# Kernel optimization log

Measured on AMD Instinct MI355X. Metric: run time of the kernel, lower is better.

## Reference

```python
import jax, jax.numpy as jnp
import numpy as np

S = 128           # seq_len
B = 256           # input_bits (bits per token, also neurons per head)
H = 16            # num_heads
NB = 12           # n_bits_per_neuron -> LUT size 2^12
PB = 7            # relative-position bits = ceil(log2(max_seq_len))
HEAD_IN = 2 * B + PB   # concat(query, key, rel_pos_bits) = 519
THRESH = H // 2


def setup_inputs() -> dict:
    key = jax.random.key(0)
    k1, k2, k3 = jax.random.split(key, 3)
    tokens = jax.random.randint(k1, (S, B), 0, 2, dtype=jnp.int32)           # binary token bits
    memory = jax.random.normal(k2, (H, B, 2 ** NB), dtype=jnp.float32)       # RAM LUT contents per head/neuron
    connections = jax.random.randint(k3, (H, B, NB), 0, HEAD_IN, dtype=jnp.int32)  # per-neuron input-bit wiring
    return {"tokens": tokens, "memory": memory, "connections": connections}


def reference(tokens, memory, connections):
    idx = jnp.arange(S)
    rel = idx[:, None] - idx[None, :]                         # [S,S] i - j
    mask = (rel >= 0).astype(jnp.int32)                        # causal mask (j <= i)
    relc = jnp.clip(rel, 0, S - 1)
    # relative-distance binary encoding, LSB first: [S,S,PB]
    pos_bits = ((relc[..., None] >> jnp.arange(PB)) & 1).astype(jnp.int32)
    q = jnp.broadcast_to(tokens[:, None, :], (S, S, B))
    k = jnp.broadcast_to(tokens[None, :, :], (S, S, B))
    head_in = jnp.concatenate([q, k, pos_bits], axis=-1)       # [S,S,HEAD_IN]
    # RAM address per (query i, key j, head h, neuron n): pack NB wired bits, LSB first
    addr = jnp.zeros((S, S, H, B), dtype=jnp.int32)
    for b in range(NB):  # tiny fixed loop over bit planes, fully vectorized over S,S,H,B
        addr = addr + (head_in[..., connections[:, :, b]] << b)
    # LUT gather: memory[h, n, addr] -> [S,S,H,B]
    h_idx = jnp.arange(H)[:, None]
    n_idx = jnp.arange(B)[None, :]
    vals = memory[h_idx, n_idx, addr]
    bits = (vals > 0.0).astype(jnp.int32)                      # RAM neuron output bit
    # XOR accumulation over attended keys == masked sum mod 2: [S,H,B]
    head_res = jnp.sum(bits * mask[:, :, None, None], axis=1) % 2
    # majority vote across heads per bit
    ones_count = jnp.sum(head_res, axis=1)                     # [S,B]
    return (ones_count > THRESH).astype(jnp.int32)
```

## Files before the change

kernel.cpp:

```cpp
#include <hip/hip_runtime.h>


#define S 128
#define B 256
#define H 16
#define NB 12

__device__ __forceinline__ unsigned sig(unsigned x) {
    return x ^ ((x >> 3) & 0x70u) ^ ((x >> 6) & 0x70u);
}

__global__ __launch_bounds__(256, 4) void softram_kernel(
    const int* __restrict__ tokens,
    const float* __restrict__ memory,
    const int* __restrict__ connections,
    unsigned char* __restrict__ pc)
{
    const int bid  = blockIdx.x;
    const int g    = bid >> 8;
    const int n    = bid & 255;
    const int tid  = threadIdx.x;
    const int wid  = tid >> 6;
    const int hg   = g * 4 + wid;
    const int lane = tid & 63;

    __shared__ unsigned char  bytetab[4 * 4096];
    __shared__ unsigned int   tokT[8][S];
    __shared__ unsigned short akT[4][S];
    __shared__ unsigned short apt[4][S];
    __shared__ int            conns[4][NB];
    __shared__ unsigned int   parts[4][4];

    const float4* mrow = (const float4*)(memory + ((size_t)(hg * 256 + n) << 12));
    float4 va[16];
    #pragma unroll
    for (int t = 0; t < 16; ++t) va[t] = mrow[lane + 64 * t];

    {
        int i = tid >> 1, half = tid & 1;
        const int4* tp = (const int4*)tokens;
        #pragma unroll
        for (int wl = 0; wl < 4; ++wl) {
            int w = half * 4 + wl;
            unsigned v = 0;
            #pragma unroll
            for (int u = 0; u < 8; ++u) {
                int4 x = tp[i * 64 + w * 8 + u];
                v |= (unsigned)(x.x & 1) << (4 * u + 0);
                v |= (unsigned)(x.y & 1) << (4 * u + 1);
                v |= (unsigned)(x.z & 1) << (4 * u + 2);
                v |= (unsigned)(x.w & 1) << (4 * u + 3);
            }
            tokT[w][i] = v;
        }
    }
    if (tid < 4 * NB) {
        int hh = tid / NB, b = tid - hh * NB;
        conns[hh][b] = connections[(size_t)(g * 4 + hh) * (B * NB) + n * NB + b];
    }
    __syncthreads();

    unsigned qmask = 0, kmask = 0, pmask = 0;
    #pragma unroll
    for (int b = 0; b < NB; ++b) {
        int c = conns[wid][b];
        qmask |= (unsigned)(c < 256) << b;
        kmask |= (unsigned)(c >= 256 && c < 512) << b;
        pmask |= (unsigned)(c >= 512) << b;
    }
    const int qb = __popc(qmask);
    const int kb = __popc(kmask);

    unsigned char* __restrict__ bt = &bytetab[wid << 12];
    unsigned long long rlo = 0, rhi = 0;

    if (pmask == 0) {
        unsigned qcls0 = 0, qcls1 = 0;
        #pragma unroll
        for (int e = 0; e < 2; ++e) {
            int ii = lane + 64 * e;
            unsigned qc = 0, kc = 0;
            int qn = 0, kn = 0;
            #pragma unroll
            for (int b = 0; b < NB; ++b) {
                int c = conns[wid][b];
                if (c < 256) {
                    qc |= ((tokT[c >> 5][ii] >> (c & 31)) & 1u) << qn;
                    ++qn;
                } else {
                    int c2 = c - 256;
                    kc |= ((tokT[c2 >> 5][ii] >> (c2 & 31)) & 1u) << kn;
                    ++kn;
                }
            }
            akT[wid][ii] = (unsigned short)kc;
            if (e == 0) qcls0 = qc; else qcls1 = qc;
        }

        #pragma unroll
        for (int t = 0; t < 16; ++t) {
            float4 v = va[t];
            unsigned p = 4u * (unsigned)(lane + 64 * t);
            unsigned w = (unsigned)(v.x > 0.f)
                       | ((unsigned)(v.y > 0.f) << 8)
                       | ((unsigned)(v.z > 0.f) << 16)
                       | ((unsigned)(v.w > 0.f) << 24);
            *(unsigned*)&bt[sig(p)] = w;
        }

        const bool formA = (qb <= 6);
        const int SBITS  = formA ? qb : kb;
        unsigned apl = 0, aul = 0;
        {
            int scnt = 0, lcnt = 0;
            #pragma unroll
            for (int b = 0; b < NB; ++b) {
                int c = conns[wid][b];
                bool isS = formA ? (c < 256) : (c >= 256);
                if (isS) {
                    apl |= (((unsigned)lane >> scnt) & 1u) << b;
                    ++scnt;
                } else {
                    int p = SBITS + lcnt;
                    if (p < 6) apl |= (((unsigned)lane >> p) & 1u) << b;
                    else       aul |= (((unsigned)lane >> (p - 6)) & 1u) << b;
                    ++lcnt;
                }
            }
        }
        const unsigned spl  = sig(apl);
        const unsigned saul = sig(aul);
        unsigned Wlo = 0, Whi = 0;
        #pragma unroll 8
        for (int it = 0; it < 64; ++it) {
            unsigned sau  = (unsigned)__builtin_amdgcn_readlane((int)saul, it);
            unsigned bitv = bt[sau ^ spl] & 1u;
            unsigned long long Bm = __ballot(bitv != 0u);
            Wlo = (lane == it) ? (unsigned)Bm : Wlo;
            Whi = (lane == it) ? (unsigned)(Bm >> 32) : Whi;
        }

        if (formA) {
            unsigned long long A = 0, cap0 = 0, cap1 = 0;
            for (int s8 = 0; s8 < 8; ++s8) {
                uint4 uk = *(const uint4*)&akT[wid][s8 * 8];
                #pragma unroll
                for (int t = 0; t < 8; ++t) {
                    int j = s8 * 8 + t;
                    unsigned w = ((const unsigned*)&uk)[t >> 1];
                    unsigned widx = (unsigned)__builtin_amdgcn_readfirstlane(
                        (int)((w >> ((t & 1) * 16)) & 0xffffu));
                    unsigned g0 = widx << qb;
                    int lsel = (int)(g0 >> 6);
                    unsigned lo = (unsigned)__builtin_amdgcn_readlane((int)Wlo, lsel);
                    unsigned hi = (unsigned)__builtin_amdgcn_readlane((int)Whi, lsel);
                    A ^= ((((unsigned long long)hi << 32) | lo) >> (g0 & 63u));
                    cap0 = (lane == j) ? A : cap0;
                }
            }
            for (int s8 = 8; s8 < 16; ++s8) {
                uint4 uk = *(const uint4*)&akT[wid][s8 * 8];
                #pragma unroll
                for (int t = 0; t < 8; ++t) {
                    int j = s8 * 8 + t;
                    unsigned w = ((const unsigned*)&uk)[t >> 1];
                    unsigned widx = (unsigned)__builtin_amdgcn_readfirstlane(
                        (int)((w >> ((t & 1) * 16)) & 0xffffu));
                    unsigned g0 = widx << qb;
                    int lsel = (int)(g0 >> 6);
                    unsigned lo = (unsigned)__builtin_amdgcn_readlane((int)Wlo, lsel);
                    unsigned hi = (unsigned)__builtin_amdgcn_readlane((int)Whi, lsel);
                    A ^= ((((unsigned long long)hi << 32) | lo) >> (g0 & 63u));
                    cap1 = (lane == j - 64) ? A : cap1;
                }
            }
            rlo = __ballot(((cap0 >> qcls0) & 1ull) != 0ull);
            rhi = __ballot(((cap1 >> qcls1) & 1ull) != 0ull);
        } else {
            unsigned Cw = 0, cap0 = 0, cap1 = 0;
            for (int s8 = 0; s8 < 8; ++s8) {
                uint4 uk = *(const uint4*)&akT[wid][s8 * 8];
                #pragma unroll
                for (int t = 0; t < 8; ++t) {
                    int j = s8 * 8 + t;
                    unsigned w = ((const unsigned*)&uk)[t >> 1];
                    unsigned widx = (unsigned)__builtin_amdgcn_readfirstlane(
                        (int)((w >> ((t & 1) * 16)) & 0xffffu));
                    Cw ^= 1u << widx;
                    cap0 = (lane == j) ? Cw : cap0;
                }
            }
            for (int s8 = 8; s8 < 16; ++s8) {
                uint4 uk = *(const uint4*)&akT[wid][s8 * 8];
                #pragma unroll
                for (int t = 0; t < 8; ++t) {
                    int j = s8 * 8 + t;
                    unsigned w = ((const unsigned*)&uk)[t >> 1];
                    unsigned widx = (unsigned)__builtin_amdgcn_readfirstlane(
                        (int)((w >> ((t & 1) * 16)) & 0xffffu));
                    Cw ^= 1u << widx;
                    cap1 = (lane == j - 64) ? Cw : cap1;
                }
            }
            unsigned g0a = qcls0 << kb, g0b = qcls1 << kb;
            unsigned lo0 = (unsigned)__shfl((int)Wlo, (int)(g0a >> 6));
            unsigned hi0 = (unsigned)__shfl((int)Whi, (int)(g0a >> 6));
            unsigned lo1 = (unsigned)__shfl((int)Wlo, (int)(g0b >> 6));
            unsigned hi1 = (unsigned)__shfl((int)Whi, (int)(g0b >> 6));
            unsigned W0 = (unsigned)((((unsigned long long)hi0 << 32) | lo0) >> (g0a & 63u));
            unsigned W1 = (unsigned)((((unsigned long long)hi1 << 32) | lo1) >> (g0b & 63u));
            rlo = __ballot((__popc(W0 & cap0) & 1) != 0);
            rhi = __ballot((__popc(W1 & cap1) & 1) != 0);
        }
    } else {
        unsigned aqv0 = 0, aqv1 = 0;
        #pragma unroll
        for (int e = 0; e < 2; ++e) {
            int ii = lane + 64 * e;
            unsigned aq = 0, ak = 0, ap = 0;
            #pragma unroll
            for (int b = 0; b < NB; ++b) {
                int c = conns[wid][b];
                if (c < 256) {
                    aq |= ((tokT[c >> 5][ii] >> (c & 31)) & 1u) << b;
                } else if (c < 512) {
                    int c2 = c - 256;
                    ak |= ((tokT[c2 >> 5][ii] >> (c2 & 31)) & 1u) << b;
                } else {
                    ap |= (((unsigned)ii >> (c - 512)) & 1u) << b;
                }
            }
            akT[wid][ii] = (unsigned short)sig(ak);
            apt[wid][ii] = (unsigned short)sig(ap);
            if (e == 0) aqv0 = sig(aq); else aqv1 = sig(aq);
        }

        #pragma unroll
        for (int t = 0; t < 16; ++t) {
            float4 v = va[t];
            unsigned p = 4u * (unsigned)(lane + 64 * t);
            unsigned w = (unsigned)(v.x > 0.f)
                       | ((unsigned)(v.y > 0.f) << 8)
                       | ((unsigned)(v.z > 0.f) << 16)
                       | ((unsigned)(v.w > 0.f) << 24);
            *(unsigned*)&bt[sig(p)] = w;
        }

        unsigned acc0 = 0, acc1 = 0;
        for (int s8 = 0; s8 < 8; ++s8) {
            uint4 uk = *(const uint4*)&akT[wid][s8 * 8];
            #pragma unroll
            for (int t = 0; t < 8; ++t) {
                int j = s8 * 8 + t;
                unsigned w = ((const unsigned*)&uk)[t >> 1];
                unsigned akv = (w >> ((t & 1) * 16)) & 0xffffu;
                int d0 = lane - j;
                unsigned v0 = bt[aqv0 ^ akv ^ (unsigned)apt[wid][d0 & 127]] & 1u;
                acc0 ^= (d0 >= 0) ? v0 : 0u;
                int d1 = lane + 64 - j;
                unsigned v1 = bt[aqv1 ^ akv ^ (unsigned)apt[wid][d1]] & 1u;
                acc1 ^= v1;
            }
        }
        for (int s8 = 8; s8 < 16; ++s8) {
            uint4 uk = *(const uint4*)&akT[wid][s8 * 8];
            #pragma unroll
            for (int t = 0; t < 8; ++t) {
                int j = s8 * 8 + t;
                unsigned w = ((const unsigned*)&uk)[t >> 1];
                unsigned akv = (w >> ((t & 1) * 16)) & 0xffffu;
                int d1 = lane + 64 - j;
                unsigned v1 = bt[aqv1 ^ akv ^ (unsigned)apt[wid][d1 & 127]] & 1u;
                acc1 ^= (d1 >= 0) ? v1 : 0u;
            }
        }
        rlo = __ballot(acc0 != 0u);
        rhi = __ballot(acc1 != 0u);
    }

    if (lane == 0) {
        parts[wid][0] = (unsigned)rlo;
        parts[wid][1] = (unsigned)(rlo >> 32);
        parts[wid][2] = (unsigned)rhi;
        parts[wid][3] = (unsigned)(rhi >> 32);
    }
    __syncthreads();

    if (tid < S) {
        int i = tid, tot = 0;
        #pragma unroll
        for (int hh = 0; hh < 4; ++hh)
            tot += (parts[hh][i >> 5] >> (i & 31)) & 1;
        pc[((size_t)g * 256 + n) * 128 + i] = (unsigned char)tot;
    }
}

__global__ __launch_bounds__(128) void vote_kernel(
    const unsigned char* __restrict__ pc,
    int* __restrict__ out)
{
    const int n = blockIdx.x;
    const int i = threadIdx.x;
    int tot = pc[(size_t)(0 * 256 + n) * 128 + i]
            + pc[(size_t)(1 * 256 + n) * 128 + i]
            + pc[(size_t)(2 * 256 + n) * 128 + i]
            + pc[(size_t)(3 * 256 + n) * 128 + i];
    out[i * B + n] = (tot > (H / 2)) ? 1 : 0;
}

extern "C" void kernel_launch(void* const* d_in, const int* in_sizes, int n_in,
                              void* d_out, int out_size, void* d_ws, size_t ws_size,
                              hipStream_t stream) {
    const int*   tokens      = (const int*)d_in[0];
    const float* memory      = (const float*)d_in[1];
    const int*   connections = (const int*)d_in[2];
    int*         out         = (int*)d_out;
    unsigned char* pc        = (unsigned char*)d_ws;
    (void)in_sizes; (void)n_in; (void)out_size; (void)ws_size;

    softram_kernel<<<4 * B, 256, 0, stream>>>(tokens, memory, connections, pc);
    vote_kernel<<<B, 128, 0, stream>>>(pc, out);
}
```

Measured before the change: 121.8 us.

## Prepack token bits in a separate kernel and use wave XOR-prefix scans

Moves token bit-packing into a small pre-kernel that uses ballots, so each of the 1024 main blocks loads the packed bits with one int4 copy instead of repacking the whole token matrix from global memory. The serial 128-step readfirstlane/readlane accumulation over keys is replaced by a log-step XOR prefix scan with shfl_up across the wave, carrying the base value into the second half of the keys. It also uses writelane to build the LUT bit words. The cost is an extra kernel launch and a different packed bit layout that every tokT access must decode.

```diff
diff --git a/kernel.cpp b/kernel.cpp
--- a/kernel.cpp
+++ b/kernel.cpp
@@ -10,8 +10,35 @@
     return x ^ ((x >> 3) & 0x70u) ^ ((x >> 6) & 0x70u);
 }
 
+#define TW(c) ((((c) & 3) << 1) + ((c) >> 7))
+#define TP(c) (((c) >> 2) & 31)
+
+__global__ __launch_bounds__(256) void pack_kernel(
+    const int* __restrict__ tokens,
+    unsigned* __restrict__ tokP)
+{
+    const int wid  = threadIdx.x >> 6;
+    const int lane = threadIdx.x & 63;
+    const int4* tp = (const int4*)tokens;
+    #pragma unroll
+    for (int r = 0; r < 4; ++r) {
+        int i = blockIdx.x * 16 + wid * 4 + r;
+        int4 x = tp[i * 64 + lane];
+        unsigned long long B0 = __ballot((x.x & 1) != 0);
+        unsigned long long B1 = __ballot((x.y & 1) != 0);
+        unsigned long long B2 = __ballot((x.z & 1) != 0);
+        unsigned long long B3 = __ballot((x.w & 1) != 0);
+        int c = lane >> 1;
+        unsigned long long s01 = (c & 1) ? B1 : B0;
+        unsigned long long s23 = (c & 1) ? B3 : B2;
+        unsigned long long s   = (c & 2) ? s23 : s01;
+        unsigned word = (lane & 1) ? (unsigned)(s >> 32) : (unsigned)s;
+        if (lane < 8) tokP[lane * 128 + i] = word;
+    }
+}
+
 __global__ __launch_bounds__(256, 4) void softram_kernel(
-    const int* __restrict__ tokens,
+    const unsigned* __restrict__ tokP,
     const float* __restrict__ memory,
     const int* __restrict__ connections,
     unsigned char* __restrict__ pc)
@@ -24,10 +51,10 @@
     const int hg   = g * 4 + wid;
     const int lane = tid & 63;
 
-    __shared__ unsigned char  bytetab[4 * 4096];
-    __shared__ unsigned int   tokT[8][S];
-    __shared__ unsigned short akT[4][S];
-    __shared__ unsigned short apt[4][S];
+    __shared__ __align__(16) unsigned char  bytetab[4 * 4096];
+    __shared__ __align__(16) unsigned int   tokT[8 * S];
+    __shared__ __align__(16) unsigned short akT[4][S];
+    __shared__ __align__(16) unsigned short apt[4][S];
     __shared__ int            conns[4][NB];
     __shared__ unsigned int   parts[4][4];
 
@@ -36,24 +63,7 @@
     #pragma unroll
     for (int t = 0; t < 16; ++t) va[t] = mrow[lane + 64 * t];
 
-    {
-        int i = tid >> 1, half = tid & 1;
-        const int4* tp = (const int4*)tokens;
-        #pragma unroll
-        for (int wl = 0; wl < 4; ++wl) {
-            int w = half * 4 + wl;
-            unsigned v = 0;
-            #pragma unroll
-            for (int u = 0; u < 8; ++u) {
-                int4 x = tp[i * 64 + w * 8 + u];
-                v |= (unsigned)(x.x & 1) << (4 * u + 0);
-                v |= (unsigned)(x.y & 1) << (4 * u + 1);
-                v |= (unsigned)(x.z & 1) << (4 * u + 2);
-                v |= (unsigned)(x.w & 1) << (4 * u + 3);
-            }
-            tokT[w][i] = v;
-        }
-    }
+    ((int4*)tokT)[tid] = ((const int4*)tokP)[tid];
     if (tid < 4 * NB) {
         int hh = tid / NB, b = tid - hh * NB;
         conns[hh][b] = connections[(size_t)(g * 4 + hh) * (B * NB) + n * NB + b];
@@ -75,7 +85,7 @@
     unsigned long long rlo = 0, rhi = 0;
 
     if (pmask == 0) {
-        unsigned qcls0 = 0, qcls1 = 0;
+        unsigned qclsA = 0, qclsB = 0;
         #pragma unroll
         for (int e = 0; e < 2; ++e) {
             int ii = lane + 64 * e;
@@ -85,16 +95,16 @@
             for (int b = 0; b < NB; ++b) {
                 int c = conns[wid][b];
                 if (c < 256) {
-                    qc |= ((tokT[c >> 5][ii] >> (c & 31)) & 1u) << qn;
+                    qc |= ((tokT[TW(c) * S + ii] >> TP(c)) & 1u) << qn;
                     ++qn;
                 } else {
                     int c2 = c - 256;
-                    kc |= ((tokT[c2 >> 5][ii] >> (c2 & 31)) & 1u) << kn;
+                    kc |= ((tokT[TW(c2) * S + ii] >> TP(c2)) & 1u) << kn;
                     ++kn;
                 }
             }
             akT[wid][ii] = (unsigned short)kc;
-            if (e == 0) qcls0 = qc; else qcls1 = qc;
+            if (e == 0) qclsA = qc; else qclsB = qc;
         }
 
         #pragma unroll
@@ -136,81 +146,62 @@
             unsigned sau  = (unsigned)__builtin_amdgcn_readlane((int)saul, it);
             unsigned bitv = bt[sau ^ spl] & 1u;
             unsigned long long Bm = __ballot(bitv != 0u);
+#if __has_builtin(__builtin_amdgcn_writelane)
+            Wlo = (unsigned)__builtin_amdgcn_writelane((int)(unsigned)Bm, it, (int)Wlo);
+            Whi = (unsigned)__builtin_amdgcn_writelane((int)(unsigned)(Bm >> 32), it, (int)Whi);
+#else
             Wlo = (lane == it) ? (unsigned)Bm : Wlo;
             Whi = (lane == it) ? (unsigned)(Bm >> 32) : Whi;
-        }
+#endif
+        }
+        const unsigned long long Wfull = ((unsigned long long)Whi << 32) | Wlo;
 
         if (formA) {
-            unsigned long long A = 0, cap0 = 0, cap1 = 0;
-            for (int s8 = 0; s8 < 8; ++s8) {
-                uint4 uk = *(const uint4*)&akT[wid][s8 * 8];
-                #pragma unroll
-                for (int t = 0; t < 8; ++t) {
-                    int j = s8 * 8 + t;
-                    unsigned w = ((const unsigned*)&uk)[t >> 1];
-                    unsigned widx = (unsigned)__builtin_amdgcn_readfirstlane(
-                        (int)((w >> ((t & 1) * 16)) & 0xffffu));
-                    unsigned g0 = widx << qb;
-                    int lsel = (int)(g0 >> 6);
-                    unsigned lo = (unsigned)__builtin_amdgcn_readlane((int)Wlo, lsel);
-                    unsigned hi = (unsigned)__builtin_amdgcn_readlane((int)Whi, lsel);
-                    A ^= ((((unsigned long long)hi << 32) | lo) >> (g0 & 63u));
-                    cap0 = (lane == j) ? A : cap0;
-                }
-            }
-            for (int s8 = 8; s8 < 16; ++s8) {
-                uint4 uk = *(const uint4*)&akT[wid][s8 * 8];
-                #pragma unroll
-                for (int t = 0; t < 8; ++t) {
-                    int j = s8 * 8 + t;
-                    unsigned w = ((const unsigned*)&uk)[t >> 1];
-                    unsigned widx = (unsigned)__builtin_amdgcn_readfirstlane(
-                        (int)((w >> ((t & 1) * 16)) & 0xffffu));
-                    unsigned g0 = widx << qb;
-                    int lsel = (int)(g0 >> 6);
-                    unsigned lo = (unsigned)__builtin_amdgcn_readlane((int)Wlo, lsel);
-                    unsigned hi = (unsigned)__builtin_amdgcn_readlane((int)Whi, lsel);
-                    A ^= ((((unsigned long long)hi << 32) | lo) >> (g0 & 63u));
-                    cap1 = (lane == j - 64) ? A : cap1;
-                }
-            }
-            rlo = __ballot(((cap0 >> qcls0) & 1ull) != 0ull);
-            rhi = __ballot(((cap1 >> qcls1) & 1ull) != 0ull);
+            unsigned kclsA = akT[wid][lane];
+            unsigned g0 = kclsA << qb;
+            unsigned long long V = __shfl(Wfull, (int)(g0 >> 6)) >> (g0 & 63u);
+            #pragma unroll
+            for (int d = 1; d < 64; d <<= 1) {
+                unsigned long long u = __shfl_up(V, (unsigned)d);
+                V ^= (lane >= d) ? u : 0ull;
+            }
+            rlo = __ballot(((V >> qclsA) & 1ull) != 0ull);
+            const unsigned long long Abase = __shfl(V, 63);
+
+            unsigned kclsB = akT[wid][64 + lane];
+            unsigned g1 = kclsB << qb;
+            unsigned long long V1 = __shfl(Wfull, (int)(g1 >> 6)) >> (g1 & 63u);
+            #pragma unroll
+            for (int d = 1; d < 64; d <<= 1) {
+                unsigned long long u = __shfl_up(V1, (unsigned)d);
+                V1 ^= (lane >= d) ? u : 0ull;
+            }
+            V1 ^= Abase;
+            rhi = __ballot(((V1 >> qclsB) & 1ull) != 0ull);
         } else {
-            unsigned Cw = 0, cap0 = 0, cap1 = 0;
-            for (int s8 = 0; s8 < 8; ++s8) {
-                uint4 uk = *(const uint4*)&akT[wid][s8 * 8];
-                #pragma unroll
-                for (int t = 0; t < 8; ++t) {
-                    int j = s8 * 8 + t;
-                    unsigned w = ((const unsigned*)&uk)[t >> 1];
-                    unsigned widx = (unsigned)__builtin_amdgcn_readfirstlane(
-                        (int)((w >> ((t & 1) * 16)) & 0xffffu));
-                    Cw ^= 1u << widx;
-                    cap0 = (lane == j) ? Cw : cap0;
-                }
-            }
-            for (int s8 = 8; s8 < 16; ++s8) {
-                uint4 uk = *(const uint4*)&akT[wid][s8 * 8];
-                #pragma unroll
-                for (int t = 0; t < 8; ++t) {
-                    int j = s8 * 8 + t;
-                    unsigned w = ((const unsigned*)&uk)[t >> 1];
-                    unsigned widx = (unsigned)__builtin_amdgcn_readfirstlane(
-                        (int)((w >> ((t & 1) * 16)) & 0xffffu));
-                    Cw ^= 1u << widx;
-                    cap1 = (lane == j - 64) ? Cw : cap1;
-                }
-            }
-            unsigned g0a = qcls0 << kb, g0b = qcls1 << kb;
-            unsigned lo0 = (unsigned)__shfl((int)Wlo, (int)(g0a >> 6));
-            unsigned hi0 = (unsigned)__shfl((int)Whi, (int)(g0a >> 6));
-            unsigned lo1 = (unsigned)__shfl((int)Wlo, (int)(g0b >> 6));
-            unsigned hi1 = (unsigned)__shfl((int)Whi, (int)(g0b >> 6));
-            unsigned W0 = (unsigned)((((unsigned long long)hi0 << 32) | lo0) >> (g0a & 63u));
-            unsigned W1 = (unsigned)((((unsigned long long)hi1 << 32) | lo1) >> (g0b & 63u));
-            rlo = __ballot((__popc(W0 & cap0) & 1) != 0);
-            rhi = __ballot((__popc(W1 & cap1) & 1) != 0);
+            unsigned kclsA = akT[wid][lane];
+            unsigned C = 1u << kclsA;
+            #pragma unroll
+            for (int d = 1; d < 64; d <<= 1) {
+                unsigned u = __shfl_up(C, (unsigned)d);
+                C ^= (lane >= d) ? u : 0u;
+            }
+            unsigned g0a = qclsA << kb;
+            unsigned W0 = (unsigned)(__shfl(Wfull, (int)(g0a >> 6)) >> (g0a & 63u));
+            rlo = __ballot((__popc(W0 & C) & 1) != 0);
+            const unsigned Cbase = __shfl(C, 63);
+
+            unsigned kclsB = akT[wid][64 + lane];
+            unsigned C1 = 1u << kclsB;
+            #pragma unroll
+            for (int d = 1; d < 64; d <<= 1) {
+                unsigned u = __shfl_up(C1, (unsigned)d);
+                C1 ^= (lane >= d) ? u : 0u;
+            }
+            C1 ^= Cbase;
+            unsigned g0b = qclsB << kb;
+            unsigned W1 = (unsigned)(__shfl(Wfull, (int)(g0b >> 6)) >> (g0b & 63u));
+            rhi = __ballot((__popc(W1 & C1) & 1) != 0);
         }
     } else {
         unsigned aqv0 = 0, aqv1 = 0;
@@ -222,10 +213,10 @@
             for (int b = 0; b < NB; ++b) {
                 int c = conns[wid][b];
                 if (c < 256) {
-                    aq |= ((tokT[c >> 5][ii] >> (c & 31)) & 1u) << b;
+                    aq |= ((tokT[TW(c) * S + ii] >> TP(c)) & 1u) << b;
                 } else if (c < 512) {
                     int c2 = c - 256;
-                    ak |= ((tokT[c2 >> 5][ii] >> (c2 & 31)) & 1u) << b;
+                    ak |= ((tokT[TW(c2) * S + ii] >> TP(c2)) & 1u) << b;
                 } else {
                     ap |= (((unsigned)ii >> (c - 512)) & 1u) << b;
                 }
@@ -316,8 +307,10 @@
     const int*   connections = (const int*)d_in[2];
     int*         out         = (int*)d_out;
     unsigned char* pc        = (unsigned char*)d_ws;
+    unsigned*      tokP      = (unsigned*)((char*)d_ws + 4 * 256 * 128);
     (void)in_sizes; (void)n_in; (void)out_size; (void)ws_size;
 
-    softram_kernel<<<4 * B, 256, 0, stream>>>(tokens, memory, connections, pc);
+    pack_kernel<<<8, 256, 0, stream>>>(tokens, tokP);
+    softram_kernel<<<4 * B, 256, 0, stream>>>(tokP, memory, connections, pc);
     vote_kernel<<<B, 128, 0, stream>>>(pc, out);
 }
```

After: 110.0 us. 9.7% less time.
